# Kernel optimization log

Measured on AMD Instinct MI355X. Metric: run time of the kernel, lower is better.

Reference implementation:

```python
import jax, jax.numpy as jnp
import numpy as np

N_NODES, IN_DIM, HID, N_CLS, N_T = 4096, 512, 256, 128, 20


def _odefunc(x, A, Wt, bt):
    # X' = relu(Linear(A @ X)); dropout=0.0 so it is the identity
    return jax.nn.relu((A @ x) @ Wt.T + bt)


def _rk4_traj(vt, x0, A, Wt, bt):
    # torchdiffeq 'rk4' = fixed-grid 3/8-rule RK4 stepping between consecutive vt points
    f = lambda y: _odefunc(y, A, Wt, bt)  # autonomous: t unused by ODEFunc

    def step(x, dt):
        k1 = f(x)
        k2 = f(x + dt * k1 / 3.0)
        k3 = f(x + dt * (k2 - k1 / 3.0))
        k4 = f(x + dt * (k1 - k2 + k3))
        xn = x + dt * (k1 + 3.0 * k2 + 3.0 * k3 + k4) / 8.0
        return xn, xn

    dts = vt[1:] - vt[:-1]
    _, ys = jax.lax.scan(step, x0, dts)
    return jnp.concatenate([x0[None], ys], axis=0)  # [T, N, H]


def setup_inputs() -> dict:
    key = jax.random.key(0)
    ks = jax.random.split(key, 8)
    vt = jnp.arange(N_T, dtype=jnp.float32) * 0.05  # increasing time ticks, horizon ~1.0
    x = jax.random.normal(ks[0], (N_NODES, IN_DIM), dtype=jnp.float32)
    # row-scaled dense adjacency (torch.mm dense path); spectral scale ~O(1)
    A = jax.random.uniform(ks[1], (N_NODES, N_NODES), dtype=jnp.float32) / N_NODES
    W1 = jax.random.normal(ks[2], (HID, IN_DIM), dtype=jnp.float32) / np.sqrt(IN_DIM)
    b1 = jnp.zeros((HID,), dtype=jnp.float32)
    W2 = jax.random.normal(ks[3], (HID, HID), dtype=jnp.float32) / np.sqrt(HID)
    b2 = jnp.zeros((HID,), dtype=jnp.float32)
    Wt = jax.random.normal(ks[4], (HID, HID), dtype=jnp.float32) * (0.5 / np.sqrt(HID))
    bt = jnp.zeros((HID,), dtype=jnp.float32)
    Wo = jax.random.normal(ks[5], (N_CLS, HID), dtype=jnp.float32) / np.sqrt(HID)
    bo = jnp.zeros((N_CLS,), dtype=jnp.float32)
    return {"vt": vt, "x": x, "A": A, "W1": W1, "b1": b1, "W2": W2,
            "b2": b2, "Wt": Wt, "bt": bt, "Wo": Wo, "bo": bo}


def reference(vt, x, A, W1, b1, W2, b2, Wt, bt, Wo, bo):
    # input_layer: Linear -> Tanh -> Linear (dropout = 0.0 elsewhere)
    h = jnp.tanh(x @ W1.T + b1) @ W2.T + b2            # [N, H]
    traj = _rk4_traj(vt, h, A, Wt, bt)                 # [T, N, H] (terminal=False -> full trajectory)
    return traj @ Wo.T + bo                            # [T, N, C]
```

## Files before the change

### kernel.cpp

```cpp
#include <hip/hip_runtime.h>
#include <stdint.h>

typedef __bf16 bf16;
typedef bf16 bf16x8 __attribute__((ext_vector_type(8)));
typedef float f32x4 __attribute__((ext_vector_type(4)));
typedef uint32_t u32;
typedef unsigned long long u64;
typedef unsigned char u8;

#define NN   4096
#define HID  256
#define NCLS 128

__device__ __forceinline__ void gload16(const void* g, void* l) {
  __builtin_amdgcn_global_load_lds((const __attribute__((address_space(1))) u32*)g,
                                   (__attribute__((address_space(3))) u32*)l, 16, 0, 0);
}

__global__ void convf2b(const float* __restrict__ s, bf16* __restrict__ d, int n) {
  int i = (blockIdx.x * blockDim.x + threadIdx.x) * 4;
  if (i >= n) return;
  f32x4 v = *(const f32x4*)(s + i);
  bf16 o[4] = {(bf16)v[0], (bf16)v[1], (bf16)v[2], (bf16)v[3]};
  *(u64*)(d + i) = *(u64*)o;
}

__global__ void convAf8(const float* __restrict__ s, u8* __restrict__ d, int n) {
  int i = (blockIdx.x * blockDim.x + threadIdx.x) * 4;
  if (i >= n) return;
  f32x4 v = *(const f32x4*)(s + i);
  u32 pk = __builtin_amdgcn_cvt_pk_fp8_f32(v[0] * 4096.f, v[1] * 4096.f, 0, false);
  pk = __builtin_amdgcn_cvt_pk_fp8_f32(v[2] * 4096.f, v[3] * 4096.f, pk, true);
  *(u32*)(d + i) = pk;
}

__device__ __forceinline__ f32x4 ksplit_reduce(char* smem, f32x4 acc[2][2],
                                               int kw, int sw, int hh, int rl) {
  float* fs = (float*)smem;
  #pragma unroll
  for (int q = 0; q < 4; ++q) {
    const int src = (kw < q) ? kw : kw - 1;
    float* dst = fs + ((q * 3 + src) * 2 + sw) * 272;
    const int mf = q >> 1, nf = q & 1;
    if (q != kw) {
      #pragma unroll
      for (int j = 0; j < 4; ++j) dst[(hh * 4 + j) * 17 + rl] = acc[mf][nf][j];
    }
  }
  asm volatile("s_waitcnt lgkmcnt(0)" ::: "memory");
  __builtin_amdgcn_s_barrier();
  f32x4 r;
  if (kw == 0)      r = acc[0][0];
  else if (kw == 1) r = acc[0][1];
  else if (kw == 2) r = acc[1][0];
  else              r = acc[1][1];
  #pragma unroll
  for (int src = 0; src < 3; ++src) {
    const float* sp = fs + ((kw * 3 + src) * 2 + sw) * 272;
    #pragma unroll
    for (int j = 0; j < 4; ++j) r[j] += sp[(hh * 4 + j) * 17 + rl];
  }
  return r;
}

__global__ __launch_bounds__(512, 2) void gemmf8(
    const u8* __restrict__ Ag,
    const u8* __restrict__ Bg,
    bf16* __restrict__ Cb)
{
  __shared__ __align__(16) char smem[73728];
  const int tid = threadIdx.x;
  const int l = tid & 63, wv = tid >> 6;
  const int kw = wv & 3, sw = wv >> 2;
  const int rl = l & 15, hh = l >> 4;

  const int chunk = gridDim.x >> 3;
  const int sb = (blockIdx.x & 7) * chunk + (blockIdx.x >> 3);
  const int m0 = (sb >> 3) * 64, n0 = (sb & 7) * 32;

  const bool isB = wv >= 4;
  const int w4 = wv & 3;
  const int rlo = l >> 4;
  const int gq = l & 15;
  const int rowbase = isB ? n0 + w4 * 8 : m0 + w4 * 16;
  const u8* sGbase = (isB ? Bg : Ag) + (size_t)rowbase * 4096;
  const int c0 = (gq ^ rlo) << 4;
  const int c1 = (gq ^ (rlo + 4)) << 4;
  const int stoff = isB ? 16384 + w4 * 2048 : w4 * 4096;

  f32x4 acc[2][2];
  #pragma unroll
  for (int i = 0; i < 2; ++i)
    #pragma unroll
    for (int j = 0; j < 2; ++j) acc[i][j] = (f32x4){0.f, 0.f, 0.f, 0.f};

  auto stage = [&](int buf, int t) {
    char* base = smem + buf * 24576 + stoff;
    const u8* g = sGbase + (size_t)rlo * 4096 + t * 256;
    gload16(g + c0,                      base);
    gload16(g + (size_t)4  * 4096 + c1,  base + 1024);
    if (!isB) {
      gload16(g + (size_t)8  * 4096 + c0, base + 2048);
      gload16(g + (size_t)12 * 4096 + c1, base + 3072);
    }
  };

  auto compute = [&](int buf) {
    const char* As = smem + buf * 24576;
    const char* Bs = As + 16384;
    #pragma unroll
    for (int ks = 0; ks < 2; ++ks) {
      const int g0 = (kw * 2 + ks) * 2 + (hh >> 1);
      const int co = ((g0 ^ (rl & 7)) << 4) + (hh & 1) * 8;
      u64 a0 = *(const u64*)(As + (sw * 32 + rl +  0) * 256 + co);
      u64 a1 = *(const u64*)(As + (sw * 32 + rl + 16) * 256 + co);
      u64 b0 = *(const u64*)(Bs + (rl +  0) * 256 + co);
      u64 b1 = *(const u64*)(Bs + (rl + 16) * 256 + co);
      __builtin_amdgcn_s_setprio(1);
      acc[0][0] = __builtin_amdgcn_mfma_f32_16x16x32_fp8_fp8((long)a0, (long)b0, acc[0][0], 0, 0, 0);
      acc[0][1] = __builtin_amdgcn_mfma_f32_16x16x32_fp8_fp8((long)a0, (long)b1, acc[0][1], 0, 0, 0);
      acc[1][0] = __builtin_amdgcn_mfma_f32_16x16x32_fp8_fp8((long)a1, (long)b0, acc[1][0], 0, 0, 0);
      acc[1][1] = __builtin_amdgcn_mfma_f32_16x16x32_fp8_fp8((long)a1, (long)b1, acc[1][1], 0, 0, 0);
      __builtin_amdgcn_s_setprio(0);
    }
  };

  stage(0, 0); stage(1, 1);
  int cur = 0, pre = 2;
  for (int t = 0; t < 16; ++t) {
    if (t < 15) {
      if (!isB) { asm volatile("s_waitcnt vmcnt(4)" ::: "memory"); }
      else      { asm volatile("s_waitcnt vmcnt(2)" ::: "memory"); }
    } else       { asm volatile("s_waitcnt vmcnt(0)" ::: "memory"); }
    __builtin_amdgcn_sched_barrier(0);
    __builtin_amdgcn_s_barrier();
    __builtin_amdgcn_sched_barrier(0);
    if (t + 2 < 16) stage(pre, t + 2);
    compute(cur);
    cur = (cur == 2) ? 0 : cur + 1;
    pre = (pre == 2) ? 0 : pre + 1;
  }
  __builtin_amdgcn_s_barrier();
  __builtin_amdgcn_sched_barrier(0);

  f32x4 o = ksplit_reduce(smem, acc, kw, sw, hh, rl);
  const int row0 = m0 + sw * 32 + (kw >> 1) * 16 + hh * 4;
  const int col  = n0 + (kw & 1) * 16 + rl;
  #pragma unroll
  for (int r = 0; r < 4; ++r)
    Cb[(row0 + r) * HID + col] = (bf16)(o[r] * 2.44140625e-4f);
}

template<int EPI>
__global__ __launch_bounds__(512, 2) void gemmbf(
    const bf16* __restrict__ Ag, int lda,
    const bf16* __restrict__ Bg, int ldb,
    int Ntiles, int K,
    const float* __restrict__ bias,
    float* __restrict__ outf,
    bf16* __restrict__ outb,
    u8* __restrict__ ybt,
    float* __restrict__ xbuf,
    const float* __restrict__ kk1,
    const float* __restrict__ kk2,
    const float* __restrict__ kk3,
    const float* __restrict__ vt, int step)
{
  __shared__ __align__(16) char smem[49152];
  const int tid = threadIdx.x;
  const int l = tid & 63, wv = tid >> 6;
  const int kw = wv & 3, sw = wv >> 2;
  const int rl = l & 15, hh = l >> 4;

  const int chunk = gridDim.x >> 3;
  const int sb = (blockIdx.x & 7) * chunk + (blockIdx.x >> 3);
  const int mtile = sb / Ntiles;
  const int ntile = sb - mtile * Ntiles;
  const int m0 = mtile * 64, n0 = ntile * 32;

  const bool isB = wv >= 4;
  const int w4 = wv & 3;
  const int rlo = l >> 4, gq = l & 15;
  const size_t ldby = (size_t)(isB ? ldb : lda) * 2;
  const int grow = (isB ? n0 + w4 * 8 : m0 + w4 * 16) + rlo;
  const char* sGb = (const char*)(isB ? (const void*)Bg : (const void*)Ag)
                    + (size_t)grow * ldby;
  const int c0 = (gq ^ rlo) << 4;
  const int c1 = (gq ^ (rlo + 4)) << 4;
  const int stoff = isB ? 16384 + w4 * 2048 : w4 * 4096;

  f32x4 acc[2][2];
  #pragma unroll
  for (int i = 0; i < 2; ++i)
    #pragma unroll
    for (int j = 0; j < 2; ++j) acc[i][j] = (f32x4){0.f, 0.f, 0.f, 0.f};

  auto stage = [&](int buf, int t) {
    char* base = smem + buf * 24576 + stoff;
    const char* g = sGb + (size_t)t * 256;
    gload16(g + c0,            base);
    gload16(g + 4 * ldby + c1, base + 1024);
    if (!isB) {
      gload16(g +  8 * ldby + c0, base + 2048);
      gload16(g + 12 * ldby + c1, base + 3072);
    }
  };

  const int ca = ((kw * 4 + hh) ^ (rl & 7)) << 4;
  auto compute = [&](int buf) {
    const char* As = smem + buf * 24576;
    const char* Bs = As + 16384;
    bf16x8 a0 = *(const bf16x8*)(As + (sw * 32 + rl +  0) * 256 + ca);
    bf16x8 a1 = *(const bf16x8*)(As + (sw * 32 + rl + 16) * 256 + ca);
    bf16x8 b0 = *(const bf16x8*)(Bs + (rl +  0) * 256 + ca);
    bf16x8 b1 = *(const bf16x8*)(Bs + (rl + 16) * 256 + ca);
    __builtin_amdgcn_s_setprio(1);
    acc[0][0] = __builtin_amdgcn_mfma_f32_16x16x32_bf16(a0, b0, acc[0][0], 0, 0, 0);
    acc[0][1] = __builtin_amdgcn_mfma_f32_16x16x32_bf16(a0, b1, acc[0][1], 0, 0, 0);
    acc[1][0] = __builtin_amdgcn_mfma_f32_16x16x32_bf16(a1, b0, acc[1][0], 0, 0, 0);
    acc[1][1] = __builtin_amdgcn_mfma_f32_16x16x32_bf16(a1, b1, acc[1][1], 0, 0, 0);
    __builtin_amdgcn_s_setprio(0);
  };

  const int nmac = K >> 7;
  stage(0, 0);
  asm volatile("s_waitcnt vmcnt(0)" ::: "memory");
  __builtin_amdgcn_s_barrier();
  int cur = 0;
  for (int t = 0; t < nmac; ++t) {
    if (t + 1 < nmac) stage(cur ^ 1, t + 1);
    compute(cur);
    asm volatile("s_waitcnt vmcnt(0)" ::: "memory");
    __builtin_amdgcn_sched_barrier(0);
    __builtin_amdgcn_s_barrier();
    cur ^= 1;
  }
  __builtin_amdgcn_sched_barrier(0);

  f32x4 o = ksplit_reduce(smem, acc, kw, sw, hh, rl);
  const int row0 = m0 + sw * 32 + (kw >> 1) * 16 + hh * 4;
  const int col  = n0 + (kw & 1) * 16 + rl;

  float dtv = 0.f;
  if constexpr (EPI >= 3 && EPI <= 6) dtv = vt[step + 1] - vt[step];

  if constexpr (EPI == 1) {
    #pragma unroll
    for (int r = 0; r < 4; ++r)
      outb[(row0 + r) * HID + col] = (bf16)tanhf(o[r] + bias[col]);
  } else if constexpr (EPI == 2) {
    float yv[4];
    #pragma unroll
    for (int r = 0; r < 4; ++r) {
      float v = o[r] + bias[col];
      xbuf[(row0 + r) * HID + col] = v;
      outb[(row0 + r) * HID + col] = (bf16)v;
      yv[r] = v;
    }
    u32 pk = __builtin_amdgcn_cvt_pk_fp8_f32(yv[0], yv[1], 0, false);
    pk = __builtin_amdgcn_cvt_pk_fp8_f32(yv[2], yv[3], pk, true);
    *(u32*)(ybt + (size_t)col * NN + row0) = pk;
  } else if constexpr (EPI >= 3 && EPI <= 6) {
    float yv[4];
    #pragma unroll
    for (int r = 0; r < 4; ++r) {
      const int idx = (row0 + r) * HID + col;
      float v = fmaxf(o[r] + bias[col], 0.f);
      float xv = xbuf[idx];
      float y;
      if constexpr (EPI == 3)      { outf[idx] = v; y = xv + dtv * (1.f/3.f) * v; }
      else if constexpr (EPI == 4) { outf[idx] = v; y = xv + dtv * (v - kk1[idx] * (1.f/3.f)); }
      else if constexpr (EPI == 5) { outf[idx] = v; y = xv + dtv * (kk1[idx] - kk2[idx] + v); }
      else {
        float xn = xv + dtv * 0.125f * (kk1[idx] + 3.f*kk2[idx] + 3.f*kk3[idx] + v);
        xbuf[idx] = xn;
        outb[idx] = (bf16)xn;
        y = xn;
      }
      yv[r] = y;
    }
    u32 pk = __builtin_amdgcn_cvt_pk_fp8_f32(yv[0], yv[1], 0, false);
    pk = __builtin_amdgcn_cvt_pk_fp8_f32(yv[2], yv[3], pk, true);
    *(u32*)(ybt + (size_t)col * NN + row0) = pk;
  } else {
    #pragma unroll
    for (int r = 0; r < 4; ++r)
      outf[(size_t)(row0 + r) * NCLS + col] = o[r] + bias[col];
  }
}

extern "C" void kernel_launch(void* const* d_in, const int* in_sizes, int n_in,
                              void* d_out, int out_size, void* d_ws, size_t ws_size,
                              hipStream_t stream)
{
  const float* vt = (const float*)d_in[0];
  const float* x  = (const float*)d_in[1];
  const float* A  = (const float*)d_in[2];
  const float* W1 = (const float*)d_in[3];
  const float* b1 = (const float*)d_in[4];
  const float* W2 = (const float*)d_in[5];
  const float* b2 = (const float*)d_in[6];
  const float* Wt = (const float*)d_in[7];
  const float* bt = (const float*)d_in[8];
  const float* Wo = (const float*)d_in[9];
  const float* bo = (const float*)d_in[10];
  float* out = (float*)d_out;

  char* p = (char*)d_ws;
  auto carve = [&](size_t n) { char* r = p; p += (n + 255) & ~(size_t)255; return r; };
  u8*   A8  = (u8*)carve((size_t)4096 * 4096);
  bf16* xb  = (bf16*)carve((size_t)4096 * 512 * 2);
  bf16* W1b = (bf16*)carve((size_t)256 * 512 * 2);
  bf16* W2b = (bf16*)carve((size_t)256 * 256 * 2);
  bf16* Wtb = (bf16*)carve((size_t)256 * 256 * 2);
  bf16* Wob = (bf16*)carve((size_t)128 * 256 * 2);
  bf16* T1b = (bf16*)carve((size_t)4096 * 256 * 2);
  bf16* Cb  = (bf16*)carve((size_t)4096 * 256 * 2);
  u8*   Y8  = (u8*)carve((size_t)256 * 4096);
  float* xs = (float*)carve((size_t)4096 * 256 * 4);
  float* k1 = (float*)carve((size_t)4096 * 256 * 4);
  float* k2 = (float*)carve((size_t)4096 * 256 * 4);
  float* k3 = (float*)carve((size_t)4096 * 256 * 4);
  size_t base_need = (size_t)(p - (char*)d_ws);
  const size_t trajBytes = (size_t)20 * 4096 * 256 * 2;
  bool big = (ws_size >= base_need + trajBytes);
  bf16* traj = (bf16*)carve(big ? trajBytes : (size_t)4096 * 256 * 2);

  convAf8<<<16384, 256, 0, stream>>>(A,  A8,  16777216);
  convf2b<<<2048,  256, 0, stream>>>(x,  xb,  2097152);
  convf2b<<<128,   256, 0, stream>>>(W1, W1b, 131072);
  convf2b<<<64,    256, 0, stream>>>(W2, W2b, 65536);
  convf2b<<<64,    256, 0, stream>>>(Wt, Wtb, 65536);
  convf2b<<<32,    256, 0, stream>>>(Wo, Wob, 32768);

  gemmbf<1><<<512, 512, 0, stream>>>(xb, 512, W1b, 512, 8, 512, b1,
      nullptr, T1b, nullptr, nullptr, nullptr, nullptr, nullptr, vt, 0);
  gemmbf<2><<<512, 512, 0, stream>>>(T1b, 256, W2b, 256, 8, 256, b2,
      nullptr, traj, Y8, xs, nullptr, nullptr, nullptr, vt, 0);
  if (!big)
    gemmbf<7><<<256, 512, 0, stream>>>(traj, 256, Wob, 256, 4, 256, bo,
        out, nullptr, nullptr, nullptr, nullptr, nullptr, nullptr, vt, 0);

  for (int t = 0; t < 19; ++t) {
    bf16* slot = big ? (traj + (size_t)(t + 1) * 4096 * 256) : traj;
    gemmf8<<<512, 512, 0, stream>>>(A8, Y8, Cb);
    gemmbf<3><<<512, 512, 0, stream>>>(Cb, 256, Wtb, 256, 8, 256, bt,
        k1, nullptr, Y8, xs, nullptr, nullptr, nullptr, vt, t);
    gemmf8<<<512, 512, 0, stream>>>(A8, Y8, Cb);
    gemmbf<4><<<512, 512, 0, stream>>>(Cb, 256, Wtb, 256, 8, 256, bt,
        k2, nullptr, Y8, xs, k1, nullptr, nullptr, vt, t);
    gemmf8<<<512, 512, 0, stream>>>(A8, Y8, Cb);
    gemmbf<5><<<512, 512, 0, stream>>>(Cb, 256, Wtb, 256, 8, 256, bt,
        k3, nullptr, Y8, xs, k1, k2, nullptr, vt, t);
    gemmf8<<<512, 512, 0, stream>>>(A8, Y8, Cb);
    gemmbf<6><<<512, 512, 0, stream>>>(Cb, 256, Wtb, 256, 8, 256, bt,
        nullptr, slot, Y8, xs, k1, k2, k3, vt, t);
    if (!big)
      gemmbf<7><<<256, 512, 0, stream>>>(traj, 256, Wob, 256, 4, 256, bo,
          out + (size_t)(t + 1) * 4096 * 128, nullptr, nullptr, nullptr,
          nullptr, nullptr, nullptr, vt, 0);
  }
  if (big)
    gemmbf<7><<<5120, 512, 0, stream>>>(traj, 256, Wob, 256, 4, 256, bo,
        out, nullptr, nullptr, nullptr, nullptr, nullptr, nullptr, vt, 0);
}
```

Baseline: 1.468 ms.

## Fuse A@Y fp8 GEMM with Wt projection and RK4 epilogue per stage

Replaces each pair of launches per RK4 stage (the fp8 A@Y GEMM writing a bf16 intermediate, then the bf16 Wt GEMM with the RK stage epilogue) with a single kernel. Each block owns 16 node rows across all 256 hidden columns and keeps the A@Y result in shared memory. It then loads Wt into LDS, runs the second GEMM and applies the RK update. Y8 is ping-ponged between two buffers, because a block now writes its output while other blocks may still be reading the input. This removes a launch and the round trip of the intermediate C through global memory, but uses 256 blocks with 136KB of LDS and narrow 16-row M tiles, so occupancy drops and B (Y8) is re-read from L2 by every block.

```diff
diff --git a/kernel.cpp b/kernel.cpp
--- a/kernel.cpp
+++ b/kernel.cpp
@@ -34,6 +34,154 @@
   *(u32*)(d + i) = pk;
 }
 
+template<int EPI>
+__global__ __launch_bounds__(512, 2) void fstep(
+    const u8* __restrict__ A8,
+    const u8* __restrict__ Y8i,
+    const bf16* __restrict__ Wtb,
+    const float* __restrict__ bt,
+    float* __restrict__ xs,
+    float* __restrict__ kc,
+    const float* __restrict__ k1,
+    const float* __restrict__ k2,
+    const float* __restrict__ k3,
+    bf16* __restrict__ trajslot,
+    u8* __restrict__ Y8o,
+    const float* __restrict__ vt, int step)
+{
+  __shared__ __align__(16) char smem[139264];
+  const int tid = threadIdx.x;
+  const int l = tid & 63, wv = tid >> 6;
+  const int rl = l & 15, hh = l >> 4;
+
+  const int sb = (blockIdx.x & 7) * 32 + (blockIdx.x >> 3);
+  const int m0 = sb * 16;
+
+  const int r8 = l >> 3, g8 = l & 7;
+  const u8* srcB = Y8i + (size_t)(wv * 32 + r8) * 4096 + ((g8 ^ r8) << 4);
+  const u8* srcA = A8 + (size_t)(m0 + wv * 8 + r8) * 4096 + ((g8 ^ r8) << 4);
+
+  f32x4 acc0 = {0.f, 0.f, 0.f, 0.f}, acc1 = {0.f, 0.f, 0.f, 0.f};
+
+  auto stage1 = [&](int buf, int t) {
+    char* base = smem + buf * 34816;
+    char* Bb = base + 2048 + wv * 4096;
+    const u8* gB = srcB + t * 128;
+    gload16(gB,             Bb);
+    gload16(gB +  8 * 4096, Bb + 1024);
+    gload16(gB + 16 * 4096, Bb + 2048);
+    gload16(gB + 24 * 4096, Bb + 3072);
+    if (wv < 2) gload16(srcA + (size_t)t * 128, base + wv * 1024);
+  };
+
+  auto compute1 = [&](int buf) {
+    const char* Ab = smem + buf * 34816;
+    const char* Bb = Ab + 2048;
+    #pragma unroll
+    for (int ks = 0; ks < 4; ++ks) {
+      const int g0 = ks * 2 + (hh >> 1);
+      const int co = ((g0 ^ (rl & 7)) << 4) + (hh & 1) * 8;
+      u64 a0 = *(const u64*)(Ab + rl * 128 + co);
+      u64 b0 = *(const u64*)(Bb + (wv * 32 + rl) * 128 + co);
+      u64 b1 = *(const u64*)(Bb + (wv * 32 + 16 + rl) * 128 + co);
+      __builtin_amdgcn_s_setprio(1);
+      acc0 = __builtin_amdgcn_mfma_f32_16x16x32_fp8_fp8((long)a0, (long)b0, acc0, 0, 0, 0);
+      acc1 = __builtin_amdgcn_mfma_f32_16x16x32_fp8_fp8((long)a0, (long)b1, acc1, 0, 0, 0);
+      __builtin_amdgcn_s_setprio(0);
+    }
+  };
+
+  stage1(0, 0); stage1(1, 1);
+  int cur = 0, pre = 2;
+  for (int t = 0; t < 32; ++t) {
+    if (t < 31) {
+      if (wv < 2) { asm volatile("s_waitcnt vmcnt(5)" ::: "memory"); }
+      else        { asm volatile("s_waitcnt vmcnt(4)" ::: "memory"); }
+    } else        { asm volatile("s_waitcnt vmcnt(0)" ::: "memory"); }
+    __builtin_amdgcn_sched_barrier(0);
+    __builtin_amdgcn_s_barrier();
+    __builtin_amdgcn_sched_barrier(0);
+    if (t + 2 < 32) stage1(pre, t + 2);
+    compute1(cur);
+    cur = (cur == 2) ? 0 : cur + 1;
+    pre = (pre == 2) ? 0 : pre + 1;
+  }
+  __builtin_amdgcn_s_barrier();
+  __builtin_amdgcn_sched_barrier(0);
+
+  #pragma unroll
+  for (int f = 0; f < 2; ++f) {
+    const int c = wv * 32 + f * 16 + rl;
+    const f32x4 a = f ? acc1 : acc0;
+    #pragma unroll
+    for (int j = 0; j < 4; ++j) {
+      const int row = hh * 4 + j;
+      const int off = (((c >> 3) ^ (row & 7)) << 4) + (c & 7) * 2;
+      *(bf16*)(smem + row * 512 + off) = (bf16)(a[j] * 2.44140625e-4f);
+    }
+  }
+  {
+    const int r2 = l >> 5, g32 = l & 31;
+    char* Wl = smem + 8192 + wv * 16384;
+    #pragma unroll
+    for (int i = 0; i < 16; ++i) {
+      const int sg = g32 ^ ((i & 3) * 2 + r2);
+      gload16((const char*)Wtb + (size_t)(wv * 32 + i * 2 + r2) * 512 + sg * 16,
+              Wl + i * 1024);
+    }
+  }
+  asm volatile("s_waitcnt vmcnt(0) lgkmcnt(0)" ::: "memory");
+  __builtin_amdgcn_sched_barrier(0);
+  __builtin_amdgcn_s_barrier();
+  __builtin_amdgcn_sched_barrier(0);
+
+  f32x4 z0 = {0.f, 0.f, 0.f, 0.f}, z1 = {0.f, 0.f, 0.f, 0.f};
+  const char* Cl = smem;
+  const char* Wl = smem + 8192;
+  #pragma unroll
+  for (int ks = 0; ks < 8; ++ks) {
+    const int g = ks * 4 + hh;
+    const int co = ((g ^ (rl & 7)) << 4);
+    bf16x8 a  = *(const bf16x8*)(Cl + rl * 512 + co);
+    bf16x8 b0 = *(const bf16x8*)(Wl + (wv * 32 + rl) * 512 + co);
+    bf16x8 b1 = *(const bf16x8*)(Wl + (wv * 32 + 16 + rl) * 512 + co);
+    __builtin_amdgcn_s_setprio(1);
+    z0 = __builtin_amdgcn_mfma_f32_16x16x32_bf16(a, b0, z0, 0, 0, 0);
+    z1 = __builtin_amdgcn_mfma_f32_16x16x32_bf16(a, b1, z1, 0, 0, 0);
+    __builtin_amdgcn_s_setprio(0);
+  }
+
+  const float dtv = vt[step + 1] - vt[step];
+  #pragma unroll
+  for (int f = 0; f < 2; ++f) {
+    const int c = wv * 32 + f * 16 + rl;
+    const f32x4 z = f ? z1 : z0;
+    const float btc = bt[c];
+    float yv[4];
+    #pragma unroll
+    for (int j = 0; j < 4; ++j) {
+      const int node = m0 + hh * 4 + j;
+      const int idx = node * HID + c;
+      const float v = fmaxf(z[j] + btc, 0.f);
+      const float xv = xs[idx];
+      float y;
+      if constexpr (EPI == 3)      { kc[idx] = v; y = xv + dtv * (1.f/3.f) * v; }
+      else if constexpr (EPI == 4) { kc[idx] = v; y = xv + dtv * (v - k1[idx] * (1.f/3.f)); }
+      else if constexpr (EPI == 5) { kc[idx] = v; y = xv + dtv * (k1[idx] - k2[idx] + v); }
+      else {
+        const float xn = xv + dtv * 0.125f * (k1[idx] + 3.f*k2[idx] + 3.f*k3[idx] + v);
+        xs[idx] = xn;
+        trajslot[idx] = (bf16)xn;
+        y = xn;
+      }
+      yv[j] = y;
+    }
+    u32 pk = __builtin_amdgcn_cvt_pk_fp8_f32(yv[0], yv[1], 0, false);
+    pk = __builtin_amdgcn_cvt_pk_fp8_f32(yv[2], yv[3], pk, true);
+    *(u32*)(Y8o + (size_t)c * NN + m0 + hh * 4) = pk;
+  }
+}
+
 __device__ __forceinline__ f32x4 ksplit_reduce(char* smem, f32x4 acc[2][2],
                                                int kw, int sw, int hh, int rl) {
   float* fs = (float*)smem;
@@ -61,94 +209,6 @@
     for (int j = 0; j < 4; ++j) r[j] += sp[(hh * 4 + j) * 17 + rl];
   }
   return r;
-}
-
-__global__ __launch_bounds__(512, 2) void gemmf8(
-    const u8* __restrict__ Ag,
-    const u8* __restrict__ Bg,
-    bf16* __restrict__ Cb)
-{
-  __shared__ __align__(16) char smem[73728];
-  const int tid = threadIdx.x;
-  const int l = tid & 63, wv = tid >> 6;
-  const int kw = wv & 3, sw = wv >> 2;
-  const int rl = l & 15, hh = l >> 4;
-
-  const int chunk = gridDim.x >> 3;
-  const int sb = (blockIdx.x & 7) * chunk + (blockIdx.x >> 3);
-  const int m0 = (sb >> 3) * 64, n0 = (sb & 7) * 32;
-
-  const bool isB = wv >= 4;
-  const int w4 = wv & 3;
-  const int rlo = l >> 4;
-  const int gq = l & 15;
-  const int rowbase = isB ? n0 + w4 * 8 : m0 + w4 * 16;
-  const u8* sGbase = (isB ? Bg : Ag) + (size_t)rowbase * 4096;
-  const int c0 = (gq ^ rlo) << 4;
-  const int c1 = (gq ^ (rlo + 4)) << 4;
-  const int stoff = isB ? 16384 + w4 * 2048 : w4 * 4096;
-
-  f32x4 acc[2][2];
-  #pragma unroll
-  for (int i = 0; i < 2; ++i)
-    #pragma unroll
-    for (int j = 0; j < 2; ++j) acc[i][j] = (f32x4){0.f, 0.f, 0.f, 0.f};
-
-  auto stage = [&](int buf, int t) {
-    char* base = smem + buf * 24576 + stoff;
-    const u8* g = sGbase + (size_t)rlo * 4096 + t * 256;
-    gload16(g + c0,                      base);
-    gload16(g + (size_t)4  * 4096 + c1,  base + 1024);
-    if (!isB) {
-      gload16(g + (size_t)8  * 4096 + c0, base + 2048);
-      gload16(g + (size_t)12 * 4096 + c1, base + 3072);
-    }
-  };
-
-  auto compute = [&](int buf) {
-    const char* As = smem + buf * 24576;
-    const char* Bs = As + 16384;
-    #pragma unroll
-    for (int ks = 0; ks < 2; ++ks) {
-      const int g0 = (kw * 2 + ks) * 2 + (hh >> 1);
-      const int co = ((g0 ^ (rl & 7)) << 4) + (hh & 1) * 8;
-      u64 a0 = *(const u64*)(As + (sw * 32 + rl +  0) * 256 + co);
-      u64 a1 = *(const u64*)(As + (sw * 32 + rl + 16) * 256 + co);
-      u64 b0 = *(const u64*)(Bs + (rl +  0) * 256 + co);
-      u64 b1 = *(const u64*)(Bs + (rl + 16) * 256 + co);
-      __builtin_amdgcn_s_setprio(1);
-      acc[0][0] = __builtin_amdgcn_mfma_f32_16x16x32_fp8_fp8((long)a0, (long)b0, acc[0][0], 0, 0, 0);
-      acc[0][1] = __builtin_amdgcn_mfma_f32_16x16x32_fp8_fp8((long)a0, (long)b1, acc[0][1], 0, 0, 0);
-      acc[1][0] = __builtin_amdgcn_mfma_f32_16x16x32_fp8_fp8((long)a1, (long)b0, acc[1][0], 0, 0, 0);
-      acc[1][1] = __builtin_amdgcn_mfma_f32_16x16x32_fp8_fp8((long)a1, (long)b1, acc[1][1], 0, 0, 0);
-      __builtin_amdgcn_s_setprio(0);
-    }
-  };
-
-  stage(0, 0); stage(1, 1);
-  int cur = 0, pre = 2;
-  for (int t = 0; t < 16; ++t) {
-    if (t < 15) {
-      if (!isB) { asm volatile("s_waitcnt vmcnt(4)" ::: "memory"); }
-      else      { asm volatile("s_waitcnt vmcnt(2)" ::: "memory"); }
-    } else       { asm volatile("s_waitcnt vmcnt(0)" ::: "memory"); }
-    __builtin_amdgcn_sched_barrier(0);
-    __builtin_amdgcn_s_barrier();
-    __builtin_amdgcn_sched_barrier(0);
-    if (t + 2 < 16) stage(pre, t + 2);
-    compute(cur);
-    cur = (cur == 2) ? 0 : cur + 1;
-    pre = (pre == 2) ? 0 : pre + 1;
-  }
-  __builtin_amdgcn_s_barrier();
-  __builtin_amdgcn_sched_barrier(0);
-
-  f32x4 o = ksplit_reduce(smem, acc, kw, sw, hh, rl);
-  const int row0 = m0 + sw * 32 + (kw >> 1) * 16 + hh * 4;
-  const int col  = n0 + (kw & 1) * 16 + rl;
-  #pragma unroll
-  for (int r = 0; r < 4; ++r)
-    Cb[(row0 + r) * HID + col] = (bf16)(o[r] * 2.44140625e-4f);
 }
 
 template<int EPI>
@@ -160,11 +220,7 @@
     float* __restrict__ outf,
     bf16* __restrict__ outb,
     u8* __restrict__ ybt,
-    float* __restrict__ xbuf,
-    const float* __restrict__ kk1,
-    const float* __restrict__ kk2,
-    const float* __restrict__ kk3,
-    const float* __restrict__ vt, int step)
+    float* __restrict__ xbuf)
 {
   __shared__ __align__(16) char smem[49152];
   const int tid = threadIdx.x;
@@ -241,9 +297,6 @@
   const int row0 = m0 + sw * 32 + (kw >> 1) * 16 + hh * 4;
   const int col  = n0 + (kw & 1) * 16 + rl;
 
-  float dtv = 0.f;
-  if constexpr (EPI >= 3 && EPI <= 6) dtv = vt[step + 1] - vt[step];
-
   if constexpr (EPI == 1) {
     #pragma unroll
     for (int r = 0; r < 4; ++r)
@@ -256,28 +309,6 @@
       xbuf[(row0 + r) * HID + col] = v;
       outb[(row0 + r) * HID + col] = (bf16)v;
       yv[r] = v;
-    }
-    u32 pk = __builtin_amdgcn_cvt_pk_fp8_f32(yv[0], yv[1], 0, false);
-    pk = __builtin_amdgcn_cvt_pk_fp8_f32(yv[2], yv[3], pk, true);
-    *(u32*)(ybt + (size_t)col * NN + row0) = pk;
-  } else if constexpr (EPI >= 3 && EPI <= 6) {
-    float yv[4];
-    #pragma unroll
-    for (int r = 0; r < 4; ++r) {
-      const int idx = (row0 + r) * HID + col;
-      float v = fmaxf(o[r] + bias[col], 0.f);
-      float xv = xbuf[idx];
-      float y;
-      if constexpr (EPI == 3)      { outf[idx] = v; y = xv + dtv * (1.f/3.f) * v; }
-      else if constexpr (EPI == 4) { outf[idx] = v; y = xv + dtv * (v - kk1[idx] * (1.f/3.f)); }
-      else if constexpr (EPI == 5) { outf[idx] = v; y = xv + dtv * (kk1[idx] - kk2[idx] + v); }
-      else {
-        float xn = xv + dtv * 0.125f * (kk1[idx] + 3.f*kk2[idx] + 3.f*kk3[idx] + v);
-        xbuf[idx] = xn;
-        outb[idx] = (bf16)xn;
-        y = xn;
-      }
-      yv[r] = y;
     }
     u32 pk = __builtin_amdgcn_cvt_pk_fp8_f32(yv[0], yv[1], 0, false);
     pk = __builtin_amdgcn_cvt_pk_fp8_f32(yv[2], yv[3], pk, true);
@@ -315,8 +346,8 @@
   bf16* Wtb = (bf16*)carve((size_t)256 * 256 * 2);
   bf16* Wob = (bf16*)carve((size_t)128 * 256 * 2);
   bf16* T1b = (bf16*)carve((size_t)4096 * 256 * 2);
-  bf16* Cb  = (bf16*)carve((size_t)4096 * 256 * 2);
-  u8*   Y8  = (u8*)carve((size_t)256 * 4096);
+  u8*   Y8a = (u8*)carve((size_t)256 * 4096);
+  u8*   Y8b = (u8*)carve((size_t)256 * 4096);
   float* xs = (float*)carve((size_t)4096 * 256 * 4);
   float* k1 = (float*)carve((size_t)4096 * 256 * 4);
   float* k2 = (float*)carve((size_t)4096 * 256 * 4);
@@ -334,33 +365,34 @@
   convf2b<<<32,    256, 0, stream>>>(Wo, Wob, 32768);
 
   gemmbf<1><<<512, 512, 0, stream>>>(xb, 512, W1b, 512, 8, 512, b1,
-      nullptr, T1b, nullptr, nullptr, nullptr, nullptr, nullptr, vt, 0);
+      nullptr, T1b, nullptr, nullptr);
   gemmbf<2><<<512, 512, 0, stream>>>(T1b, 256, W2b, 256, 8, 256, b2,
-      nullptr, traj, Y8, xs, nullptr, nullptr, nullptr, vt, 0);
+      nullptr, traj, Y8a, xs);
   if (!big)
     gemmbf<7><<<256, 512, 0, stream>>>(traj, 256, Wob, 256, 4, 256, bo,
-        out, nullptr, nullptr, nullptr, nullptr, nullptr, nullptr, vt, 0);
-
+        out, nullptr, nullptr, nullptr);
+
+  u8* yin = Y8a;
+  u8* yout = Y8b;
   for (int t = 0; t < 19; ++t) {
     bf16* slot = big ? (traj + (size_t)(t + 1) * 4096 * 256) : traj;
-    gemmf8<<<512, 512, 0, stream>>>(A8, Y8, Cb);
-    gemmbf<3><<<512, 512, 0, stream>>>(Cb, 256, Wtb, 256, 8, 256, bt,
-        k1, nullptr, Y8, xs, nullptr, nullptr, nullptr, vt, t);
-    gemmf8<<<512, 512, 0, stream>>>(A8, Y8, Cb);
-    gemmbf<4><<<512, 512, 0, stream>>>(Cb, 256, Wtb, 256, 8, 256, bt,
-        k2, nullptr, Y8, xs, k1, nullptr, nullptr, vt, t);
-    gemmf8<<<512, 512, 0, stream>>>(A8, Y8, Cb);
-    gemmbf<5><<<512, 512, 0, stream>>>(Cb, 256, Wtb, 256, 8, 256, bt,
-        k3, nullptr, Y8, xs, k1, k2, nullptr, vt, t);
-    gemmf8<<<512, 512, 0, stream>>>(A8, Y8, Cb);
-    gemmbf<6><<<512, 512, 0, stream>>>(Cb, 256, Wtb, 256, 8, 256, bt,
-        nullptr, slot, Y8, xs, k1, k2, k3, vt, t);
+    fstep<3><<<256, 512, 0, stream>>>(A8, yin, Wtb, bt, xs, k1, nullptr, nullptr,
+        nullptr, nullptr, yout, vt, t);
+    { u8* tmp = yin; yin = yout; yout = tmp; }
+    fstep<4><<<256, 512, 0, stream>>>(A8, yin, Wtb, bt, xs, k2, k1, nullptr,
+        nullptr, nullptr, yout, vt, t);
+    { u8* tmp = yin; yin = yout; yout = tmp; }
+    fstep<5><<<256, 512, 0, stream>>>(A8, yin, Wtb, bt, xs, k3, k1, k2,
+        nullptr, nullptr, yout, vt, t);
+    { u8* tmp = yin; yin = yout; yout = tmp; }
+    fstep<6><<<256, 512, 0, stream>>>(A8, yin, Wtb, bt, xs, nullptr, k1, k2,
+        k3, slot, yout, vt, t);
+    { u8* tmp = yin; yin = yout; yout = tmp; }
     if (!big)
       gemmbf<7><<<256, 512, 0, stream>>>(traj, 256, Wob, 256, 4, 256, bo,
-          out + (size_t)(t + 1) * 4096 * 128, nullptr, nullptr, nullptr,
-          nullptr, nullptr, nullptr, vt, 0);
+          out + (size_t)(t + 1) * 4096 * 128, nullptr, nullptr, nullptr);
   }
   if (big)
     gemmbf<7><<<5120, 512, 0, stream>>>(traj, 256, Wob, 256, 4, 256, bo,
-        out, nullptr, nullptr, nullptr, nullptr, nullptr, nullptr, vt, 0);
-}
+        out, nullptr, nullptr, nullptr);
+}
```

After: 1.856 ms. +26.4%, slower.
